# Optimization experiments

Hardware: AMD Instinct MI355X
Metric: run time of the kernel (lower is better)

Reference implementation:

```python
import jax, jax.numpy as jnp
import numpy as np

LR = 0.01
BETA1 = 0.9
BETA2 = 0.999
EPS = 1e-08
V = 1_000_000   # num_embeddings
D = 64          # embedding_dim
N = 524_288     # number of gradient rows


def setup_inputs() -> dict:
    key = jax.random.key(0)
    k1, k2, k3, k4, k5 = jax.random.split(key, 5)
    idx = jax.random.randint(k1, (N,), 0, V)
    grad = jax.random.normal(k2, (N, D), jnp.float32)
    emb = jax.random.normal(k3, (V, D), jnp.float32)
    state_step = jnp.zeros((V,), jnp.float32)
    state_mem = jax.random.normal(k4, (V, D), jnp.float32)
    state_power = jax.random.uniform(k5, (V, D), jnp.float32)  # second moment must be >= 0
    return {"idx": idx, "grad": grad, "emb": emb,
            "state_step": state_step, "state_mem": state_mem, "state_power": state_power}


def reference(idx, grad, emb, state_step, state_mem, state_power):
    """Fused sparse-Adam update. Equivalent to torch unique+index_add dedup,
    gather of per-row Adam state, elementwise Adam math, scatter-back.
    Implemented jit-compatibly with fixed-size segment sums over the full table;
    untouched rows are masked so they are returned unchanged (same semantics
    as the scatter-only torch version)."""
    v = emb.shape[0]
    # dedup: per-row count and summed gradient (== unique + index_add)
    cnt = jax.ops.segment_sum(jnp.ones(idx.shape, jnp.float32), idx, num_segments=v)   # [V]
    gsum = jax.ops.segment_sum(grad, idx, num_segments=v)                               # [V, D]
    touched = cnt > 0
    gv = gsum / jnp.where(touched, cnt, 1.0)[:, None]  # mean gradient per unique index

    step_new = jnp.where(touched, state_step + 1.0, state_step)
    mem_new = jnp.where(touched[:, None], BETA1 * state_mem + (1.0 - BETA1) * gv, state_mem)
    pow_new = jnp.where(touched[:, None], BETA2 * state_power + (1.0 - BETA2) * gv * gv, state_power)

    # bias correction (guard denominators for untouched rows with step==0)
    d1 = jnp.where(touched, 1.0 - BETA1 ** step_new, 1.0)
    d2 = jnp.where(touched, 1.0 - BETA2 ** step_new, 1.0)
    mem_corr = mem_new / d1[:, None]
    pow_corr = pow_new / d2[:, None]

    upd = LR * mem_corr / (jnp.sqrt(pow_corr) + EPS)
    emb_new = jnp.where(touched[:, None], emb - upd, emb)
    return emb_new, step_new, mem_new, pow_new
```

## Files before the change

kernel.cpp:

```cpp
#include <hip/hip_runtime.h>

#define LR    0.01f
#define B1    0.9f
#define B2    0.999f
#define EPSL  1e-8f

#define LOG2_B1 (-0.15200309344504997f)
#define LOG2_B2 (-0.0014434251880582487f)

typedef float f4 __attribute__((ext_vector_type(4)));

__global__ void zero_cnt_kernel(int* __restrict__ cnt, int n) {
    int t = blockIdx.x * blockDim.x + threadIdx.x;
    int stride = gridDim.x * blockDim.x;
    for (int i = t; i < n; i += stride) cnt[i] = 0;
}

__global__ void count_kernel(const int* __restrict__ idx,
                             int* __restrict__ cnt,
                             int* __restrict__ rowpos, int N) {
    int i = blockIdx.x * blockDim.x + threadIdx.x;
    if (i >= N) return;
    int v = idx[i];
    rowpos[i] = atomicAdd(&cnt[v], 1);
}

__global__ void alloc_kernel(const int* __restrict__ cnt,
                             int* __restrict__ off,
                             int* __restrict__ cursor, int V) {
    __shared__ int sh[256];
    __shared__ int sh_base;
    int t = threadIdx.x;
    int i = blockIdx.x * 256 + t;
    int c = (i < V) ? cnt[i] : 0;
    sh[t] = c;
    __syncthreads();
    #pragma unroll
    for (int d = 1; d < 256; d <<= 1) {
        int add = (t >= d) ? sh[t - d] : 0;
        __syncthreads();
        sh[t] += add;
        __syncthreads();
    }
    if (t == 255) sh_base = atomicAdd(cursor, sh[255]);
    __syncthreads();
    if (i < V) off[i] = sh_base + sh[t] - c;
}

__global__ void fill_kernel(const int* __restrict__ idx,
                            const int* __restrict__ rowpos,
                            const int* __restrict__ off,
                            int* __restrict__ rowids, int N) {
    int i = blockIdx.x * blockDim.x + threadIdx.x;
    if (i >= N) return;
    int v = idx[i];
    rowids[off[v] + rowpos[i]] = i;
}

__global__ void adam_kernel(const f4* __restrict__ emb4,
                            const float* __restrict__ step_in,
                            const f4* __restrict__ mem4,
                            const f4* __restrict__ pow4,
                            const f4* __restrict__ grad4,
                            const int* __restrict__ cnt,
                            const int* __restrict__ off,
                            const int* __restrict__ rowids,
                            float* __restrict__ out,
                            int V) {
    int t = blockIdx.x * blockDim.x + threadIdx.x;
    int v = t >> 4;
    int q = t & 15;
    if (v >= V) return;

    f4*    emb_out  = (f4*)out;
    float* step_out = out + (long)V * 64;
    f4*    mem_out  = (f4*)(out + (long)V * 64 + V);
    f4*    pow_out  = mem_out + (long)V * 16;

    int c = cnt[v];
    int o = off[v];
    bool touched = (c > 0);

    f4 gs = {0.f, 0.f, 0.f, 0.f};
    for (int j = 0; j < c; ++j) {
        int r = rowids[o + j];
        f4 g = __builtin_nontemporal_load(&grad4[(long)r * 16 + q]);
        gs += g;
    }

    f4 e = __builtin_nontemporal_load(&emb4[t]);
    f4 m = __builtin_nontemporal_load(&mem4[t]);
    f4 p = __builtin_nontemporal_load(&pow4[t]);
    float s_old = step_in[v];
    float s_new = touched ? s_old + 1.f : s_old;

    float inv_c = touched ? 1.f / (float)c : 0.f;
    float d1 = touched ? 1.f - exp2f(s_new * LOG2_B1) : 1.f;
    float d2 = touched ? 1.f - exp2f(s_new * LOG2_B2) : 1.f;
    float inv_d1 = 1.f / d1;
    float inv_d2 = 1.f / d2;

    f4 m_new, p_new, e_new;
    #pragma unroll
    for (int k = 0; k < 4; ++k) {
        float gv = gs[k] * inv_c;
        float mn = touched ? B1 * m[k] + (1.f - B1) * gv : m[k];
        float pn = touched ? B2 * p[k] + (1.f - B2) * gv * gv : p[k];
        float upd = LR * (mn * inv_d1) / (sqrtf(pn * inv_d2) + EPSL);
        m_new[k] = mn;
        p_new[k] = pn;
        e_new[k] = touched ? e[k] - upd : e[k];
    }

    __builtin_nontemporal_store(e_new, &emb_out[t]);
    __builtin_nontemporal_store(m_new, &mem_out[t]);
    __builtin_nontemporal_store(p_new, &pow_out[t]);
    if (q == 0) step_out[v] = s_new;
}

extern "C" void kernel_launch(void* const* d_in, const int* in_sizes, int n_in,
                              void* d_out, int out_size, void* d_ws, size_t ws_size,
                              hipStream_t stream) {
    const int*   idx  = (const int*)  d_in[0];
    const float* grad = (const float*)d_in[1];
    const float* emb  = (const float*)d_in[2];
    const float* step = (const float*)d_in[3];
    const float* mem  = (const float*)d_in[4];
    const float* pw   = (const float*)d_in[5];

    const int N = in_sizes[0];
    const int V = in_sizes[3];

    float* out = (float*)d_out;

    int* cnt    = (int*)d_ws;
    int* cursor = cnt + V;
    int* off    = cursor + 1;
    int* rowpos = off + V;
    int* rowids = rowpos + N;

    zero_cnt_kernel<<<1024, 256, 0, stream>>>(cnt, V + 1);
    count_kernel<<<(N + 255) / 256, 256, 0, stream>>>(idx, cnt, rowpos, N);
    alloc_kernel<<<(V + 255) / 256, 256, 0, stream>>>(cnt, off, cursor, V);
    fill_kernel<<<(N + 255) / 256, 256, 0, stream>>>(idx, rowpos, off, rowids, N);
    {
        long total = (long)V * 16;
        int threads = 256;
        int blocks = (int)((total + threads - 1) / threads);
        adam_kernel<<<blocks, threads, 0, stream>>>((const f4*)emb, step,
                                                    (const f4*)mem, (const f4*)pw,
                                                    (const f4*)grad,
                                                    cnt, off, rowids, out, V);
    }
}
```

Baseline: 369.8 us.

## Fuse CSR build kernels into one cooperative kernel with grid syncs

```diff
diff --git a/kernel.cpp b/kernel.cpp
--- a/kernel.cpp
+++ b/kernel.cpp
@@ -1,4 +1,7 @@
 #include <hip/hip_runtime.h>
+#include <hip/hip_cooperative_groups.h>
+
+namespace cg = cooperative_groups;
 
 #define LR    0.01f
 #define B1    0.9f
@@ -10,51 +13,85 @@
 
 typedef float f4 __attribute__((ext_vector_type(4)));
 
-__global__ void zero_cnt_kernel(int* __restrict__ cnt, int n) {
-    int t = blockIdx.x * blockDim.x + threadIdx.x;
-    int stride = gridDim.x * blockDim.x;
-    for (int i = t; i < n; i += stride) cnt[i] = 0;
-}
+#define FUSED_BLOCKS  1024
+#define FUSED_THREADS 256
+#define FUSED_NTH     (FUSED_BLOCKS * FUSED_THREADS)
+#define ROWS_PER_TH   4
 
-__global__ void count_kernel(const int* __restrict__ idx,
-                             int* __restrict__ cnt,
-                             int* __restrict__ rowpos, int N) {
-    int i = blockIdx.x * blockDim.x + threadIdx.x;
-    if (i >= N) return;
-    int v = idx[i];
-    rowpos[i] = atomicAdd(&cnt[v], 1);
-}
+__global__ void __launch_bounds__(FUSED_THREADS)
+build_csr_kernel(const int* __restrict__ idx,
+                 int2* __restrict__ co,
+                 int*  __restrict__ rowids,
+                 int*  __restrict__ cursor,
+                 int N, int V) {
+    cg::grid_group grid = cg::this_grid();
+    const int tid = blockIdx.x * FUSED_THREADS + threadIdx.x;
 
-__global__ void alloc_kernel(const int* __restrict__ cnt,
-                             int* __restrict__ off,
-                             int* __restrict__ cursor, int V) {
-    __shared__ int sh[256];
-    __shared__ int sh_base;
-    int t = threadIdx.x;
-    int i = blockIdx.x * 256 + t;
-    int c = (i < V) ? cnt[i] : 0;
-    sh[t] = c;
-    __syncthreads();
+    for (int i = tid; i < V; i += FUSED_NTH) co[i] = make_int2(0, 0);
+    if (tid == 0) *cursor = 0;
+    __threadfence();
+    grid.sync();
+
+    int my_v[ROWS_PER_TH], my_slot[ROWS_PER_TH];
     #pragma unroll
-    for (int d = 1; d < 256; d <<= 1) {
-        int add = (t >= d) ? sh[t - d] : 0;
-        __syncthreads();
-        sh[t] += add;
-        __syncthreads();
+    for (int k = 0; k < ROWS_PER_TH; ++k) {
+        int i = tid + k * FUSED_NTH;
+        if (i < N) {
+            int v = idx[i];
+            my_v[k] = v;
+            my_slot[k] = atomicAdd(&co[v].y, 1);
+        }
     }
-    if (t == 255) sh_base = atomicAdd(cursor, sh[255]);
-    __syncthreads();
-    if (i < V) off[i] = sh_base + sh[t] - c;
-}
+    __threadfence();
+    grid.sync();
 
-__global__ void fill_kernel(const int* __restrict__ idx,
-                            const int* __restrict__ rowpos,
-                            const int* __restrict__ off,
-                            int* __restrict__ rowids, int N) {
-    int i = blockIdx.x * blockDim.x + threadIdx.x;
-    if (i >= N) return;
-    int v = idx[i];
-    rowids[off[v] + rowpos[i]] = i;
+    {
+        __shared__ int sh[FUSED_THREADS];
+        __shared__ int sh_base;
+        const int t = threadIdx.x;
+        for (int chunk = blockIdx.x; chunk * 1024 < V; chunk += gridDim.x) {
+            int base = chunk * 1024 + t * 4;
+            int c[4];
+            int s = 0;
+            #pragma unroll
+            for (int k = 0; k < 4; ++k) {
+                int i = base + k;
+                c[k] = (i < V) ? co[i].y : 0;
+                s += c[k];
+            }
+            int own = s;
+            sh[t] = s;
+            __syncthreads();
+            #pragma unroll
+            for (int d = 1; d < FUSED_THREADS; d <<= 1) {
+                int add = (t >= d) ? sh[t - d] : 0;
+                __syncthreads();
+                sh[t] += add;
+                __syncthreads();
+            }
+            if (t == FUSED_THREADS - 1) sh_base = atomicAdd(cursor, sh[FUSED_THREADS - 1]);
+            __syncthreads();
+            int pre = sh_base + sh[t] - own;
+            #pragma unroll
+            for (int k = 0; k < 4; ++k) {
+                int i = base + k;
+                if (i < V) co[i].x = pre;
+                pre += c[k];
+            }
+            __syncthreads();
+        }
+    }
+    __threadfence();
+    grid.sync();
+
+    #pragma unroll
+    for (int k = 0; k < ROWS_PER_TH; ++k) {
+        int i = tid + k * FUSED_NTH;
+        if (i < N) {
+            int o = co[my_v[k]].x;
+            rowids[o + my_slot[k]] = i;
+        }
+    }
 }
 
 __global__ void adam_kernel(const f4* __restrict__ emb4,
@@ -62,8 +99,7 @@
                             const f4* __restrict__ mem4,
                             const f4* __restrict__ pow4,
                             const f4* __restrict__ grad4,
-                            const int* __restrict__ cnt,
-                            const int* __restrict__ off,
+                            const int2* __restrict__ co,
                             const int* __restrict__ rowids,
                             float* __restrict__ out,
                             int V) {
@@ -77,8 +113,9 @@
     f4*    mem_out  = (f4*)(out + (long)V * 64 + V);
     f4*    pow_out  = mem_out + (long)V * 16;
 
-    int c = cnt[v];
-    int o = off[v];
+    int2 oc = co[v];
+    int o = oc.x;
+    int c = oc.y;
     bool touched = (c > 0);
 
     f4 gs = {0.f, 0.f, 0.f, 0.f};
@@ -121,35 +158,37 @@
 extern "C" void kernel_launch(void* const* d_in, const int* in_sizes, int n_in,
                               void* d_out, int out_size, void* d_ws, size_t ws_size,
                               hipStream_t stream) {
-    const int*   idx  = (const int*)  d_in[0];
-    const float* grad = (const float*)d_in[1];
-    const float* emb  = (const float*)d_in[2];
-    const float* step = (const float*)d_in[3];
-    const float* mem  = (const float*)d_in[4];
-    const float* pw   = (const float*)d_in[5];
+    const int*   idx_p  = (const int*)  d_in[0];
+    const float* grad_p = (const float*)d_in[1];
+    const float* emb_p  = (const float*)d_in[2];
+    const float* step_p = (const float*)d_in[3];
+    const float* mem_p  = (const float*)d_in[4];
+    const float* pw_p   = (const float*)d_in[5];
 
-    const int N = in_sizes[0];
-    const int V = in_sizes[3];
+    int N = in_sizes[0];
+    int V = in_sizes[3];
 
     float* out = (float*)d_out;
 
-    int* cnt    = (int*)d_ws;
-    int* cursor = cnt + V;
-    int* off    = cursor + 1;
-    int* rowpos = off + V;
-    int* rowids = rowpos + N;
+    int2* co     = (int2*)d_ws;
+    int*  rowids = (int*)(co + V);
+    int*  cursor = rowids + N;
 
-    zero_cnt_kernel<<<1024, 256, 0, stream>>>(cnt, V + 1);
-    count_kernel<<<(N + 255) / 256, 256, 0, stream>>>(idx, cnt, rowpos, N);
-    alloc_kernel<<<(V + 255) / 256, 256, 0, stream>>>(cnt, off, cursor, V);
-    fill_kernel<<<(N + 255) / 256, 256, 0, stream>>>(idx, rowpos, off, rowids, N);
+    {
+        void* args[] = {(void*)&idx_p, (void*)&co, (void*)&rowids,
+                        (void*)&cursor, (void*)&N, (void*)&V};
+        hipLaunchCooperativeKernel((const void*)build_csr_kernel,
+                                   dim3(FUSED_BLOCKS), dim3(FUSED_THREADS),
+                                   args, 0, stream);
+    }
+
     {
         long total = (long)V * 16;
         int threads = 256;
         int blocks = (int)((total + threads - 1) / threads);
-        adam_kernel<<<blocks, threads, 0, stream>>>((const f4*)emb, step,
-                                                    (const f4*)mem, (const f4*)pw,
-                                                    (const f4*)grad,
-                                                    cnt, off, rowids, out, V);
+        adam_kernel<<<blocks, threads, 0, stream>>>((const f4*)emb_p, step_p,
+                                                    (const f4*)mem_p, (const f4*)pw_p,
+                                                    (const f4*)grad_p,
+                                                    co, rowids, out, V);
     }
 }
```

After: 841.9 us. 2.28x slower.
